# Kernel tuning notes

Hardware: AMD Instinct MI355X
Metric: run time of the kernel (lower is better)

The kernel has to match this reference:

```python
import jax, jax.numpy as jnp
import numpy as np

B, T, D, H = 4, 2048, 1024, 16
DK = D // H


def setup_inputs() -> dict:
    key = jax.random.key(0)
    ks = jax.random.split(key, 8)
    s = 0.02
    return {
        "query": jax.random.normal(ks[0], (B, T, D), jnp.float32),
        "key": jax.random.normal(ks[1], (B, T, D), jnp.float32),
        "value": jax.random.normal(ks[2], (B, T, D), jnp.float32),
        "mask": jnp.ones((B, T, T), jnp.int32),  # 1 = attend, 0 = masked out
        "Wq": jax.random.normal(ks[3], (D, D), jnp.float32) * s,
        "bq": jnp.zeros((D,), jnp.float32),
        "Wk": jax.random.normal(ks[4], (D, D), jnp.float32) * s,
        "bk": jnp.zeros((D,), jnp.float32),
        "Wv": jax.random.normal(ks[5], (D, D), jnp.float32) * s,
        "bv": jnp.zeros((D,), jnp.float32),
        "Wo": jax.random.normal(ks[6], (D, D), jnp.float32) * s,
        "bo": jnp.zeros((D,), jnp.float32),
    }


def reference(query, key, value, mask, Wq, bq, Wk, bk, Wv, bv, Wo, bo):
    b, t1, d = query.shape
    h, dk = H, DK
    # linear projections (torch nn.Linear: x @ W.T + b), split heads
    q = (query @ Wq.T + bq).reshape(b, t1, h, dk).transpose(0, 2, 1, 3)  # b h t1 dk
    k = (key @ Wk.T + bk).reshape(b, -1, h, dk).transpose(0, 2, 1, 3)    # b h t2 dk
    v = (value @ Wv.T + bv).reshape(b, -1, h, dk).transpose(0, 2, 1, 3)  # b h t2 dk
    scores = jnp.einsum('bhqd,bhkd->bhqk', q, k) / jnp.sqrt(jnp.float32(dk))
    neg = jnp.finfo(scores.dtype).min
    m = (mask[:, None, :, :] == 0)  # b 1 t1 t2 broadcast over heads
    scores = jnp.where(m, neg, scores)
    attn = jax.nn.softmax(scores, axis=-1)
    attn = jnp.where(m, 0.0, attn)
    # dropout_rate = 0.0 -> identity
    x = jnp.einsum('bhqk,bhkd->bhqd', attn, v)
    x = x.transpose(0, 2, 1, 3).reshape(b, t1, h * dk)
    out = x @ Wo.T + bo
    return out, attn
```

## Files before the change

kernel.cpp:

```cpp
#include <hip/hip_runtime.h>
#include <hip/hip_bf16.h>
#include <stdint.h>

#define B_ 4
#define T_ 2048
#define D_ 1024
#define H_ 16
#define DK_ 64
#define LOG2E 1.44269504088896340736f
#define NEGF (-3.0e38f)

typedef __attribute__((ext_vector_type(8))) short bf16x8;
typedef __attribute__((ext_vector_type(4))) float f32x4;

#define FENCE()   asm volatile("" ::: "memory")
#define SCHEDB()  __builtin_amdgcn_sched_barrier(0)
#define SBAR()    __builtin_amdgcn_s_barrier()
#define WAITV0()  asm volatile("s_waitcnt vmcnt(0)" ::: "memory")
#define WAITL0()  asm volatile("s_waitcnt lgkmcnt(0)" ::: "memory")
#define WAITLV8() asm volatile("s_waitcnt lgkmcnt(0) vmcnt(8)" ::: "memory")

__device__ inline unsigned short f2bf(float f){
  union { float f; unsigned int u; } v; v.f = f;
  return (unsigned short)((v.u + 0x7FFFu + ((v.u >> 16) & 1u)) >> 16);
}
__device__ inline unsigned int pk2(float a, float b){
  return (unsigned int)f2bf(a) | ((unsigned int)f2bf(b) << 16);
}
__device__ inline f32x4 mfma16(bf16x8 a, bf16x8 b, f32x4 c){
  return __builtin_amdgcn_mfma_f32_16x16x32_bf16(a, b, c, 0, 0, 0);
}
__device__ inline bf16x8 lds_frag(const unsigned short* base, int row, int slot){
  return *(const bf16x8*)((const char*)base + row*128 + ((slot ^ (row & 7)) << 4));
}
__device__ inline void gload16(const void* g, void* l){
  __builtin_amdgcn_global_load_lds((const __attribute__((address_space(1))) void*)g,
                                   (__attribute__((address_space(3))) void*)l, 16, 0, 0);
}
__device__ inline void stage_gl128(const unsigned short* __restrict__ g, int ld,
                                   unsigned short* lds, int wave, int lane){
#pragma unroll
  for (int i = 0; i < 4; ++i){
    int row = wave*32 + i*8 + (lane >> 3);
    int c = (lane & 7) ^ (row & 7);
    gload16(g + (size_t)row*ld + c*8, lds + (wave*32 + i*8)*64);
  }
}
__device__ inline void stage_gl64(const unsigned short* __restrict__ g, int ld,
                                  unsigned short* lds, int wave, int lane){
#pragma unroll
  for (int i = 0; i < 2; ++i){
    int row = wave*16 + i*8 + (lane >> 3);
    int c = (lane & 7) ^ (row & 7);
    gload16(g + (size_t)row*ld + c*8, lds + (wave*16 + i*8)*64);
  }
}

__global__ void pack_mask_k(const int* __restrict__ mask, unsigned long long* __restrict__ bits){
  int i = blockIdx.x * 256 + threadIdx.x;
  unsigned long long b = __ballot(mask[i] != 0);
  if ((threadIdx.x & 63) == 0) bits[i >> 6] = b;
}

__global__ void convw_k(const float* __restrict__ Wq, const float* __restrict__ Wk,
                        const float* __restrict__ Wv, const float* __restrict__ Wo,
                        unsigned short* __restrict__ dst){
  int g = blockIdx.x*256 + threadIdx.x;
  int w = g >> 17;
  int off = (g & 131071) * 8;
  const float* s = (w==0) ? Wq : (w==1) ? Wk : (w==2) ? Wv : Wo;
  float4 a = *(const float4*)(s + off);
  float4 b2 = *(const float4*)(s + off + 4);
  uint4 o;
  o.x = pk2(a.x,a.y); o.y = pk2(a.z,a.w); o.z = pk2(b2.x,b2.y); o.w = pk2(b2.z,b2.w);
  *(uint4*)(dst + (size_t)w*1048576 + off) = o;
}

__global__ void convx3_k(const float* __restrict__ q, const float* __restrict__ k,
                         const float* __restrict__ v, unsigned short* __restrict__ dst){
  int g = blockIdx.x*256 + threadIdx.x;
  int w = g >> 20;
  int off = (g & 1048575) * 8;
  const float* s = (w==0) ? q : (w==1) ? k : v;
  float4 a = *(const float4*)(s + off);
  float4 b2 = *(const float4*)(s + off + 4);
  uint4 o;
  o.x = pk2(a.x,a.y); o.y = pk2(a.z,a.w); o.z = pk2(b2.x,b2.y); o.w = pk2(b2.z,b2.w);
  *(uint4*)(dst + (size_t)w*8388608 + off) = o;
}

template<int MODE>
__global__ __launch_bounds__(256, 2)
void gemm_nt(const unsigned short* __restrict__ A, const unsigned short* __restrict__ W,
             const float* __restrict__ bias, void* __restrict__ C, float oscale)
{
  __shared__ __align__(16) unsigned short As[128*64];
  __shared__ __align__(16) unsigned short Bs[128*64];
  const int tid = threadIdx.x, lane = tid & 63, wave = tid >> 6;
  const int lcol = lane & 15, lgrp = lane >> 4;
  const int mtile = blockIdx.y, ntile = blockIdx.x;
  const int wm = (wave & 1) * 64, wn = (wave >> 1) * 64;
  f32x4 acc[4][4] = {};
#pragma unroll 1
  for (int kt = 0; kt < 16; ++kt){
    if constexpr (MODE == 2){
      int m0 = mtile*128; int b = m0 >> 11; int t0 = m0 & 2047;
      const unsigned short* xbase = A + (((size_t)(b*16 + kt)*2048 + t0) << 6);
      stage_gl128(xbase, 64, As, wave, lane);
    } else {
      stage_gl128(A + (size_t)(mtile*128)*1024 + kt*64, 1024, As, wave, lane);
    }
    stage_gl128(W + (size_t)(ntile*128)*1024 + kt*64, 1024, Bs, wave, lane);
    __syncthreads();
    bf16x8 af[4][2], bfr[4][2];
#pragma unroll
    for (int mi=0;mi<4;mi++)
#pragma unroll
      for (int kh=0;kh<2;kh++)
        af[mi][kh] = lds_frag(As, wm + mi*16 + lcol, kh*4 + lgrp);
#pragma unroll
    for (int ni=0;ni<4;ni++)
#pragma unroll
      for (int kh=0;kh<2;kh++)
        bfr[ni][kh] = lds_frag(Bs, wn + ni*16 + lcol, kh*4 + lgrp);
    __builtin_amdgcn_s_setprio(1);
#pragma unroll
    for (int mi=0;mi<4;mi++)
#pragma unroll
      for (int ni=0;ni<4;ni++)
#pragma unroll
        for (int kh=0;kh<2;kh++)
          acc[mi][ni] = mfma16(af[mi][kh], bfr[ni][kh], acc[mi][ni]);
    __builtin_amdgcn_s_setprio(0);
    __syncthreads();
  }
#pragma unroll
  for (int mi=0;mi<4;mi++){
#pragma unroll
    for (int ni=0;ni<4;ni++){
      int n = ntile*128 + wn + ni*16 + lcol;
#pragma unroll
      for (int r=0;r<4;r++){
        int m = mtile*128 + wm + mi*16 + lgrp*4 + r;
        float v = acc[mi][ni][r];
        if constexpr (MODE == 0){
          v = (v + bias[n]) * oscale;
          int bb = m >> 11, t = m & 2047, hh = n >> 6, dk = n & 63;
          ((unsigned short*)C)[(((size_t)(bb*H_ + hh)*T_ + t) << 6) + dk] = f2bf(v);
        } else if constexpr (MODE == 1){
          v += bias[m];
          int bb = n >> 11, t = n & 2047, hh = m >> 6, dk = m & 63;
          ((unsigned short*)C)[(((size_t)(bb*H_ + hh)*DK_ + dk) << 11) + t] = f2bf(v);
        } else {
          v += bias[n];
          ((float*)C)[(size_t)m*D_ + n] = v;
        }
      }
    }
  }
}

__global__ __launch_bounds__(256, 3)
void attn_k(const unsigned short* __restrict__ Qbh, const unsigned short* __restrict__ Kbh,
            const unsigned short* __restrict__ Vt, const unsigned long long* __restrict__ mbits,
            float* __restrict__ attn, unsigned short* __restrict__ Xq)
{
  __shared__ __align__(16) unsigned short Ks[2][64*64];
  __shared__ __align__(16) unsigned short Vts[2][64*64];
  __shared__ __align__(16) unsigned short Ps[128*64];
  __shared__ int s_mall;
  const int tid = threadIdx.x, lane = tid & 63, wave = tid >> 6;
  const int lcol = lane & 15, lgrp = lane >> 4;
  const int id = blockIdx.x;
  const int bh = (id & 7)*8 + ((id >> 3) >> 4);
  const int qt = (id >> 3) & 15;
  const int b = bh >> 4;
  const int q0 = qt * 128;

  const unsigned short* Kbase = Kbh + ((size_t)bh*T_) * DK_;
  const unsigned short* Vbase = Vt + (size_t)bh*DK_*T_;

  {
    const ulonglong2* mp = (const ulonglong2*)(mbits + ((size_t)b*T_ + q0)*32) + tid*8;
    unsigned long long macc = ~0ull;
#pragma unroll
    for (int i=0;i<8;i++){ ulonglong2 v = mp[i]; macc &= v.x & v.y; }
    if (tid == 0) s_mall = 1;
    __syncthreads();
    if (!__all(macc == ~0ull) && (lane == 0)) atomicAnd(&s_mall, 0);
  }

  stage_gl128(Qbh + ((size_t)bh*T_ + q0)*DK_, 64, Ps, wave, lane);
  stage_gl64(Kbase, 64, Ks[0], wave, lane);
  __syncthreads();
  const bool mall = (s_mall != 0);
  bf16x8 qf[2][2];
#pragma unroll
  for (int h=0;h<2;h++)
#pragma unroll
    for (int kh=0;kh<2;kh++)
      qf[h][kh] = lds_frag(Ps, h*64 + wave*16 + lcol, kh*4 + lgrp);

  const int qr = wave*16 + lcol;
  const unsigned long long* mrp0 = mbits + ((size_t)b*T_ + q0 + qr)*32;
  const unsigned long long* mrp1 = mrp0 + 64*32;
  const int bit0 = lgrp*4;

  float ls0 = 0.f, ls1 = 0.f;

#pragma unroll 1
  for (int kv=0; kv<32; ++kv){
    if (kv < 31) stage_gl64(Kbase + (size_t)(kv+1)*64*DK_, 64, Ks[(kv+1)&1], wave, lane);
    const unsigned short* kcur = Ks[kv&1];
    f32x4 sf[2][4] = {};
    __builtin_amdgcn_s_setprio(1);
#pragma unroll
    for (int kh=0;kh<2;kh++){
      bf16x8 kf[4];
#pragma unroll
      for (int kb=0;kb<4;kb++) kf[kb] = lds_frag(kcur, kb*16 + lcol, kh*4 + lgrp);
#pragma unroll
      for (int h=0;h<2;h++)
#pragma unroll
        for (int kb=0;kb<4;kb++)
          sf[h][kb] = mfma16(kf[kb], qf[h][kh], sf[h][kb]);
    }
    __builtin_amdgcn_s_setprio(0);
    if (mall){
      float p0 = 0.f, p1 = 0.f;
#pragma unroll
      for (int kb=0;kb<4;kb++)
#pragma unroll
        for (int r=0;r<4;r++){ p0 += exp2f(sf[0][kb][r]); p1 += exp2f(sf[1][kb][r]); }
      ls0 += p0; ls1 += p1;
    } else {
      unsigned long long w0 = mrp0[kv], w1 = mrp1[kv];
#pragma unroll
      for (int kb=0;kb<4;kb++)
#pragma unroll
        for (int r=0;r<4;r++){
          int bit = kb*16 + bit0 + r;
          ls0 += exp2f(((w0 >> bit) & 1ull) ? sf[0][kb][r] : NEGF);
          ls1 += exp2f(((w1 >> bit) & 1ull) ? sf[1][kb][r] : NEGF);
        }
    }
    __syncthreads();
  }

  ls0 += __shfl_xor(ls0, 16); ls0 += __shfl_xor(ls0, 32);
  ls1 += __shfl_xor(ls1, 16); ls1 += __shfl_xor(ls1, 32);
  const float mmr0 = (ls0 > 0.f) ? __log2f(ls0) : 3.0e38f;
  const float mmr1 = (ls1 > 0.f) ? __log2f(ls1) : 3.0e38f;

  f32x4 oacc[2][4] = {};

  stage_gl64(Kbase, 64, Ks[0], wave, lane);
  stage_gl64(Vbase, T_, Vts[0], wave, lane);

  if (mall){
    WAITV0(); SCHEDB(); SBAR();
#pragma unroll 1
    for (int kv=0; kv<32; ++kv){
      if (kv < 31){
        stage_gl64(Kbase + (size_t)(kv+1)*64*DK_, 64, Ks[(kv+1)&1], wave, lane);
        stage_gl64(Vbase + (size_t)(kv+1)*64, T_, Vts[(kv+1)&1], wave, lane);
      }
      FENCE(); SCHEDB();
      const unsigned short* kcur = Ks[kv&1];
      f32x4 sf[2][4] = {};
      __builtin_amdgcn_s_setprio(1);
#pragma unroll
      for (int kh=0;kh<2;kh++){
        bf16x8 kf[4];
#pragma unroll
        for (int kb=0;kb<4;kb++) kf[kb] = lds_frag(kcur, kb*16 + lcol, kh*4 + lgrp);
#pragma unroll
        for (int h=0;h<2;h++)
#pragma unroll
          for (int kb=0;kb<4;kb++)
            sf[h][kb] = mfma16(kf[kb], qf[h][kh], sf[h][kb]);
      }
      __builtin_amdgcn_s_setprio(0);
      const int sw = qr & 7;
#pragma unroll
      for (int h=0;h<2;h++){
        const float mm = h ? mmr1 : mmr0;
        float* arow = attn + ((size_t)bh*T_ + q0 + h*64 + qr)*T_ + kv*64 + bit0;
        char* prow = (char*)Ps + (h*64 + qr)*128 + ((lgrp & 1) << 3);
#pragma unroll
        for (int kb=0;kb<4;kb++){
          float p0 = exp2f(sf[h][kb][0] - mm);
          float p1 = exp2f(sf[h][kb][1] - mm);
          float p2 = exp2f(sf[h][kb][2] - mm);
          float p3 = exp2f(sf[h][kb][3] - mm);
          f32x4 st = {p0, p1, p2, p3};
          __builtin_nontemporal_store(st, (f32x4*)(arow + kb*16));
          uint2 pb;
          pb.x = pk2(p0, p1);
          pb.y = pk2(p2, p3);
          *(uint2*)(prow + ((((kb << 1) | (lgrp >> 1)) ^ sw) << 4)) = pb;
        }
      }
      WAITL0(); SCHEDB(); SBAR();
      const unsigned short* vcur = Vts[kv&1];
      __builtin_amdgcn_s_setprio(1);
#pragma unroll
      for (int kh=0;kh<2;kh++){
        bf16x8 af = lds_frag(vcur, wave*16 + lcol, kh*4 + lgrp);
#pragma unroll
        for (int h=0;h<2;h++)
#pragma unroll
          for (int qb=0;qb<4;qb++)
            oacc[h][qb] = mfma16(af, lds_frag(Ps + h*4096, qb*16 + lcol, kh*4 + lgrp), oacc[h][qb]);
      }
      __builtin_amdgcn_s_setprio(0);
      WAITLV8(); SCHEDB(); SBAR();
    }
  } else {
    __syncthreads();
#pragma unroll 1
    for (int kv=0; kv<32; ++kv){
      if (kv < 31){
        stage_gl64(Kbase + (size_t)(kv+1)*64*DK_, 64, Ks[(kv+1)&1], wave, lane);
        stage_gl64(Vbase + (size_t)(kv+1)*64, T_, Vts[(kv+1)&1], wave, lane);
      }
      unsigned long long wm_[2] = {mrp0[kv], mrp1[kv]};
      const unsigned short* kcur = Ks[kv&1];
      f32x4 sf[2][4] = {};
#pragma unroll
      for (int kh=0;kh<2;kh++){
        bf16x8 kf[4];
#pragma unroll
        for (int kb=0;kb<4;kb++) kf[kb] = lds_frag(kcur, kb*16 + lcol, kh*4 + lgrp);
#pragma unroll
        for (int h=0;h<2;h++)
#pragma unroll
          for (int kb=0;kb<4;kb++)
            sf[h][kb] = mfma16(kf[kb], qf[h][kh], sf[h][kb]);
      }
      const int sw = qr & 7;
#pragma unroll
      for (int h=0;h<2;h++){
        const float mm = h ? mmr1 : mmr0;
        unsigned long long w = wm_[h];
        float* arow = attn + ((size_t)bh*T_ + q0 + h*64 + qr)*T_ + kv*64 + bit0;
        char* prow = (char*)Ps + (h*64 + qr)*128 + ((lgrp & 1) << 3);
#pragma unroll
        for (int kb=0;kb<4;kb++){
          float p0 = exp2f(sf[h][kb][0] - mm);
          float p1 = exp2f(sf[h][kb][1] - mm);
          float p2 = exp2f(sf[h][kb][2] - mm);
          float p3 = exp2f(sf[h][kb][3] - mm);
          p0 = ((w >> (kb*16 + bit0    )) & 1ull) ? p0 : 0.f;
          p1 = ((w >> (kb*16 + bit0 + 1)) & 1ull) ? p1 : 0.f;
          p2 = ((w >> (kb*16 + bit0 + 2)) & 1ull) ? p2 : 0.f;
          p3 = ((w >> (kb*16 + bit0 + 3)) & 1ull) ? p3 : 0.f;
          f32x4 st = {p0, p1, p2, p3};
          __builtin_nontemporal_store(st, (f32x4*)(arow + kb*16));
          uint2 pb;
          pb.x = pk2(p0, p1);
          pb.y = pk2(p2, p3);
          *(uint2*)(prow + ((((kb << 1) | (lgrp >> 1)) ^ sw) << 4)) = pb;
        }
      }
      __syncthreads();
      const unsigned short* vcur = Vts[kv&1];
#pragma unroll
      for (int kh=0;kh<2;kh++){
        bf16x8 af = lds_frag(vcur, wave*16 + lcol, kh*4 + lgrp);
#pragma unroll
        for (int h=0;h<2;h++)
#pragma unroll
          for (int qb=0;qb<4;qb++)
            oacc[h][qb] = mfma16(af, lds_frag(Ps + h*4096, qb*16 + lcol, kh*4 + lgrp), oacc[h][qb]);
      }
      __syncthreads();
    }
  }

  unsigned short* Es = (unsigned short*)Ks;
#pragma unroll 1
  for (int h=0;h<2;h++){
    __syncthreads();
#pragma unroll
    for (int qb=0;qb<4;qb++){
      uint2 pv;
      pv.x = pk2(oacc[h][qb][0], oacc[h][qb][1]);
      pv.y = pk2(oacc[h][qb][2], oacc[h][qb][3]);
      *(uint2*)(Es + (qb*16 + lcol)*68 + wave*16 + lgrp*4) = pv;
    }
    __syncthreads();
    unsigned short* xrow = Xq + ((size_t)bh*T_ + q0 + h*64)*DK_;
#pragma unroll
    for (int it=0; it<4; ++it){
      int idx = tid + it*256;
      int q = idx >> 4, sl = idx & 15;
      uint2 v = *(const uint2*)(Es + q*68 + sl*4);
      *(uint2*)(xrow + (size_t)q*64 + sl*4) = v;
    }
  }
}

extern "C" void kernel_launch(void* const* d_in, const int* in_sizes, int n_in,
                              void* d_out, int out_size, void* d_ws, size_t ws_size,
                              hipStream_t stream) {
  const float* query = (const float*)d_in[0];
  const float* key   = (const float*)d_in[1];
  const float* value = (const float*)d_in[2];
  const int*   mask  = (const int*)d_in[3];
  const float* Wq = (const float*)d_in[4];  const float* bq = (const float*)d_in[5];
  const float* Wk = (const float*)d_in[6];  const float* bk = (const float*)d_in[7];
  const float* Wv = (const float*)d_in[8];  const float* bv = (const float*)d_in[9];
  const float* Wo = (const float*)d_in[10]; const float* bo = (const float*)d_in[11];

  float* out  = (float*)d_out;
  float* attn = out + (size_t)B_*T_*D_;

  char* ws = (char*)d_ws;
  unsigned short* Qbh = (unsigned short*)(ws);
  unsigned short* Kbh = (unsigned short*)(ws + ((size_t)16<<20));
  unsigned short* Vt  = (unsigned short*)(ws + ((size_t)32<<20));
  unsigned long long* mb = (unsigned long long*)(ws + ((size_t)48<<20));
  unsigned short* Wbf = (unsigned short*)(ws + ((size_t)50<<20));
  unsigned short* Xbf = (unsigned short*)attn;

  pack_mask_k<<<dim3((B_*T_*T_)/256), 256, 0, stream>>>(mask, mb);
  convw_k<<<dim3(2048), 256, 0, stream>>>(Wq, Wk, Wv, Wo, Wbf);
  convx3_k<<<dim3(12288), 256, 0, stream>>>(query, key, value, Xbf);
  gemm_nt<0><<<dim3(8,64), 256, 0, stream>>>(Xbf,              Wbf,            bq, Qbh, 0.125f*LOG2E);
  gemm_nt<0><<<dim3(8,64), 256, 0, stream>>>(Xbf + 8388608,    Wbf + (1u<<20), bk, Kbh, 1.0f);
  gemm_nt<1><<<dim3(64,8), 256, 0, stream>>>(Wbf + (2u<<20),   Xbf + 16777216, bv, Vt, 1.0f);
  attn_k<<<dim3(1024), 256, 0, stream>>>(Qbh, Kbh, Vt, mb, attn, Qbh);
  gemm_nt<2><<<dim3(8,64), 256, 0, stream>>>(Qbh, Wbf + (3u<<20), bo, out, 1.0f);
}
```

Before: 523.6 us.

## Merge conversion kernels, use hardware exp2 and bf16 intrinsic, raise GEMM occupancy

Fuses the weight and activation fp32-to-bf16 conversion kernels into a single launch. Replaces exp2f with the raw hardware exp2 builtin in the attention kernel. Swaps the manual round-to-nearest bf16 conversion for the HIP bf16 constructor. Raises the GEMM launch bound from 2 to 3 blocks per CU. The aim is to cut launch overhead and ALU work in softmax, at the cost of possible register spills in the GEMM and slightly different exp2 precision and handling of denormals.

```diff
diff --git a/kernel.cpp b/kernel.cpp
--- a/kernel.cpp
+++ b/kernel.cpp
@@ -21,12 +21,14 @@
 #define WAITLV8() asm volatile("s_waitcnt lgkmcnt(0) vmcnt(8)" ::: "memory")
 
 __device__ inline unsigned short f2bf(float f){
-  union { float f; unsigned int u; } v; v.f = f;
-  return (unsigned short)((v.u + 0x7FFFu + ((v.u >> 16) & 1u)) >> 16);
+  union { __hip_bfloat16 h; unsigned short u; } v;
+  v.h = __hip_bfloat16(f);
+  return v.u;
 }
 __device__ inline unsigned int pk2(float a, float b){
   return (unsigned int)f2bf(a) | ((unsigned int)f2bf(b) << 16);
 }
+__device__ inline float fexp2(float x){ return __builtin_amdgcn_exp2f(x); }
 __device__ inline f32x4 mfma16(bf16x8 a, bf16x8 b, f32x4 c){
   return __builtin_amdgcn_mfma_f32_16x16x32_bf16(a, b, c, 0, 0, 0);
 }
@@ -62,35 +64,32 @@
   if ((threadIdx.x & 63) == 0) bits[i >> 6] = b;
 }
 
-__global__ void convw_k(const float* __restrict__ Wq, const float* __restrict__ Wk,
-                        const float* __restrict__ Wv, const float* __restrict__ Wo,
-                        unsigned short* __restrict__ dst){
+__global__ void convall_k(const float* __restrict__ Wq, const float* __restrict__ Wk,
+                          const float* __restrict__ Wv, const float* __restrict__ Wo,
+                          const float* __restrict__ q, const float* __restrict__ k,
+                          const float* __restrict__ v,
+                          unsigned short* __restrict__ wdst, unsigned short* __restrict__ xdst){
   int g = blockIdx.x*256 + threadIdx.x;
-  int w = g >> 17;
-  int off = (g & 131071) * 8;
-  const float* s = (w==0) ? Wq : (w==1) ? Wk : (w==2) ? Wv : Wo;
+  const float* s; unsigned short* d; int off;
+  if (g < 524288){
+    int w = g >> 17; off = (g & 131071) * 8;
+    s = (w==0) ? Wq : (w==1) ? Wk : (w==2) ? Wv : Wo;
+    d = wdst + (size_t)w*1048576 + off;
+  } else {
+    int gg = g - 524288;
+    int w = gg >> 20; off = (gg & 1048575) * 8;
+    s = (w==0) ? q : (w==1) ? k : v;
+    d = xdst + (size_t)w*8388608 + off;
+  }
   float4 a = *(const float4*)(s + off);
   float4 b2 = *(const float4*)(s + off + 4);
   uint4 o;
   o.x = pk2(a.x,a.y); o.y = pk2(a.z,a.w); o.z = pk2(b2.x,b2.y); o.w = pk2(b2.z,b2.w);
-  *(uint4*)(dst + (size_t)w*1048576 + off) = o;
-}
-
-__global__ void convx3_k(const float* __restrict__ q, const float* __restrict__ k,
-                         const float* __restrict__ v, unsigned short* __restrict__ dst){
-  int g = blockIdx.x*256 + threadIdx.x;
-  int w = g >> 20;
-  int off = (g & 1048575) * 8;
-  const float* s = (w==0) ? q : (w==1) ? k : v;
-  float4 a = *(const float4*)(s + off);
-  float4 b2 = *(const float4*)(s + off + 4);
-  uint4 o;
-  o.x = pk2(a.x,a.y); o.y = pk2(a.z,a.w); o.z = pk2(b2.x,b2.y); o.w = pk2(b2.z,b2.w);
-  *(uint4*)(dst + (size_t)w*8388608 + off) = o;
+  *(uint4*)d = o;
 }
 
 template<int MODE>
-__global__ __launch_bounds__(256, 2)
+__global__ __launch_bounds__(256, 3)
 void gemm_nt(const unsigned short* __restrict__ A, const unsigned short* __restrict__ W,
              const float* __restrict__ bias, void* __restrict__ C, float oscale)
 {
@@ -231,7 +230,7 @@
 #pragma unroll
       for (int kb=0;kb<4;kb++)
 #pragma unroll
-        for (int r=0;r<4;r++){ p0 += exp2f(sf[0][kb][r]); p1 += exp2f(sf[1][kb][r]); }
+        for (int r=0;r<4;r++){ p0 += fexp2(sf[0][kb][r]); p1 += fexp2(sf[1][kb][r]); }
       ls0 += p0; ls1 += p1;
     } else {
       unsigned long long w0 = mrp0[kv], w1 = mrp1[kv];
@@ -240,8 +239,8 @@
 #pragma unroll
         for (int r=0;r<4;r++){
           int bit = kb*16 + bit0 + r;
-          ls0 += exp2f(((w0 >> bit) & 1ull) ? sf[0][kb][r] : NEGF);
-          ls1 += exp2f(((w1 >> bit) & 1ull) ? sf[1][kb][r] : NEGF);
+          ls0 += fexp2(((w0 >> bit) & 1ull) ? sf[0][kb][r] : NEGF);
+          ls1 += fexp2(((w1 >> bit) & 1ull) ? sf[1][kb][r] : NEGF);
         }
     }
     __syncthreads();
@@ -289,10 +288,10 @@
         char* prow = (char*)Ps + (h*64 + qr)*128 + ((lgrp & 1) << 3);
 #pragma unroll
         for (int kb=0;kb<4;kb++){
-          float p0 = exp2f(sf[h][kb][0] - mm);
-          float p1 = exp2f(sf[h][kb][1] - mm);
-          float p2 = exp2f(sf[h][kb][2] - mm);
-          float p3 = exp2f(sf[h][kb][3] - mm);
+          float p0 = fexp2(sf[h][kb][0] - mm);
+          float p1 = fexp2(sf[h][kb][1] - mm);
+          float p2 = fexp2(sf[h][kb][2] - mm);
+          float p3 = fexp2(sf[h][kb][3] - mm);
           f32x4 st = {p0, p1, p2, p3};
           __builtin_nontemporal_store(st, (f32x4*)(arow + kb*16));
           uint2 pb;
@@ -347,10 +346,10 @@
         char* prow = (char*)Ps + (h*64 + qr)*128 + ((lgrp & 1) << 3);
 #pragma unroll
         for (int kb=0;kb<4;kb++){
-          float p0 = exp2f(sf[h][kb][0] - mm);
-          float p1 = exp2f(sf[h][kb][1] - mm);
-          float p2 = exp2f(sf[h][kb][2] - mm);
-          float p3 = exp2f(sf[h][kb][3] - mm);
+          float p0 = fexp2(sf[h][kb][0] - mm);
+          float p1 = fexp2(sf[h][kb][1] - mm);
+          float p2 = fexp2(sf[h][kb][2] - mm);
+          float p3 = fexp2(sf[h][kb][3] - mm);
           p0 = ((w >> (kb*16 + bit0    )) & 1ull) ? p0 : 0.f;
           p1 = ((w >> (kb*16 + bit0 + 1)) & 1ull) ? p1 : 0.f;
           p2 = ((w >> (kb*16 + bit0 + 2)) & 1ull) ? p2 : 0.f;
@@ -425,8 +424,7 @@
   unsigned short* Xbf = (unsigned short*)attn;
 
   pack_mask_k<<<dim3((B_*T_*T_)/256), 256, 0, stream>>>(mask, mb);
-  convw_k<<<dim3(2048), 256, 0, stream>>>(Wq, Wk, Wv, Wo, Wbf);
-  convx3_k<<<dim3(12288), 256, 0, stream>>>(query, key, value, Xbf);
+  convall_k<<<dim3(14336), 256, 0, stream>>>(Wq, Wk, Wv, Wo, query, key, value, Wbf, Xbf);
   gemm_nt<0><<<dim3(8,64), 256, 0, stream>>>(Xbf,              Wbf,            bq, Qbh, 0.125f*LOG2E);
   gemm_nt<0><<<dim3(8,64), 256, 0, stream>>>(Xbf + 8388608,    Wbf + (1u<<20), bk, Kbh, 1.0f);
   gemm_nt<1><<<dim3(64,8), 256, 0, stream>>>(Wbf + (2u<<20),   Xbf + 16777216, bv, Vt, 1.0f);
```

Result: no change. 530.4 us (+1.3%).
